# Optimization experiments

Measured on AMD Instinct MI355X. Metric: run time of the kernel, lower is better.

The kernel has to match this reference:

```python
import jax, jax.numpy as jnp
import numpy as np

NUM_HEADS = 16


def rotate_half(x):
    h = x.shape[-1] // 2
    return jnp.concatenate([-x[..., h:], x[..., :h]], axis=-1)


def setup_inputs() -> dict:
    key = jax.random.key(0)
    ks = jax.random.split(key, 8)
    S, dim, hd = 8192, 1280, 80
    n_seg = 8
    hidden_states = jax.random.normal(ks[0], (S, dim), dtype=jnp.float32)
    cu_seqlens = (jnp.arange(n_seg + 1, dtype=jnp.int32) * (S // n_seg))
    ang = jax.random.uniform(ks[1], (S, hd), dtype=jnp.float32) * (2.0 * np.pi)
    cos = jnp.cos(ang)
    sin = jnp.sin(ang)
    qkv_w = jax.random.normal(ks[2], (3 * dim, dim), dtype=jnp.float32) * (dim ** -0.5)
    qkv_b = jax.random.normal(ks[3], (3 * dim,), dtype=jnp.float32) * 0.02
    proj_w = jax.random.normal(ks[4], (dim, dim), dtype=jnp.float32) * (dim ** -0.5)
    proj_b = jax.random.normal(ks[5], (dim,), dtype=jnp.float32) * 0.02
    return {"hidden_states": hidden_states, "cu_seqlens": cu_seqlens,
            "cos": cos, "sin": sin, "qkv_w": qkv_w, "qkv_b": qkv_b,
            "proj_w": proj_w, "proj_b": proj_b}


def reference(hidden_states, cu_seqlens, cos, sin, qkv_w, qkv_b, proj_w, proj_b):
    S, dim = hidden_states.shape
    H = NUM_HEADS
    hd = dim // H
    scaling = hd ** -0.5

    # qkv projection: [S, 3*dim] -> [S, 3, H, hd]
    qkv = (hidden_states @ qkv_w.T + qkv_b).reshape(S, 3, H, hd)
    q, k, v = qkv[:, 0], qkv[:, 1], qkv[:, 2]  # each [S, H, hd]

    # RoPE in float32, cos/sin broadcast over heads
    c = cos[:, None, :].astype(jnp.float32)
    s = sin[:, None, :].astype(jnp.float32)
    qf, kf = q.astype(jnp.float32), k.astype(jnp.float32)
    q = (qf * c + rotate_half(qf) * s).astype(q.dtype)
    k = (kf * c + rotate_half(kf) * s).astype(k.dtype)

    # Block-diagonal varlen attention: equal-length segments -> batch dim
    lengths = np.diff(np.asarray(cu_seqlens))
    L = int(lengths[0])
    assert (lengths == L).all(), "reference assumes uniform segment lengths"
    B = lengths.shape[0]
    qb = q.reshape(B, L, H, hd)
    kb = k.reshape(B, L, H, hd)
    vb = v.reshape(B, L, H, hd)

    scores = jnp.einsum('blhd,bmhd->bhlm', qb, kb) * scaling
    probs = jax.nn.softmax(scores.astype(jnp.float32), axis=-1).astype(scores.dtype)
    out = jnp.einsum('bhlm,bmhd->blhd', probs, vb).reshape(S, dim)

    return out @ proj_w.T + proj_b
```

## Files before the change

### kernel.cpp

```cpp
#include <hip/hip_runtime.h>
#include <math.h>

typedef _Float16 f16;
typedef _Float16 half8 __attribute__((ext_vector_type(8)));
typedef _Float16 half4v __attribute__((ext_vector_type(4)));
typedef _Float16 half2v __attribute__((ext_vector_type(2)));
typedef float floatx4 __attribute__((ext_vector_type(4)));
typedef unsigned int u32;

#define AS1 __attribute__((address_space(1)))
#define AS3 __attribute__((address_space(3)))

__device__ __forceinline__ void stage16(f16* l, const f16* g) {
    __builtin_amdgcn_global_load_lds((const AS1 u32*)g, (AS3 u32*)l, 16, 0, 0);
}

__global__ __launch_bounds__(256) void cvt_f32_f16(const float* __restrict__ in,
                                                   f16* __restrict__ out, int n4) {
    int i = blockIdx.x * blockDim.x + threadIdx.x;
    if (i >= n4) return;
    float4 v = ((const float4*)in)[i];
    half4v h = {(f16)v.x, (f16)v.y, (f16)v.z, (f16)v.w};
    ((half4v*)out)[i] = h;
}

__global__ __launch_bounds__(256) void pack_w(const float* __restrict__ Wf,
                                              f16* __restrict__ Wp) {
    const int p = blockIdx.x * 256 + threadIdx.x;
    const int lane = p & 63;
    const int j = (p >> 6) & 3;
    const int sk = p >> 8;
    const int k0 = sk % 40;
    const int slab = sk / 40;
    const int row = slab * 64 + j * 16 + (lane & 15);
    const int col = k0 * 32 + (lane >> 4) * 8;
    const float* src = Wf + (size_t)row * 1280 + col;
    float4 a = *(const float4*)src;
    float4 b = *(const float4*)(src + 4);
    half8 h = {(f16)a.x, (f16)a.y, (f16)a.z, (f16)a.w,
               (f16)b.x, (f16)b.y, (f16)b.z, (f16)b.w};
    *(half8*)(Wp + (size_t)p * 8) = h;
}

constexpr int GK = 1280;
constexpr int KT = 20;

template <int MT>
__global__ __launch_bounds__(512, 2) void gemm_bp(const f16* __restrict__ A,
                                                  const f16* __restrict__ Bp,
                                                  const float* __restrict__ bias,
                                                  f16* __restrict__ outH,
                                                  float* __restrict__ outF,
                                                  int N, int NT) {
    constexpr int M_FR = MT / 32;
    constexpr int QE = MT * 32;
    __shared__ f16 sm[2][2][QE];
    const int t = threadIdx.x;
    const int lane = t & 63, w = t >> 6;
    const int wm = w >> 2, wn = w & 3;
    const int c16 = lane & 15, quad = lane >> 4;
    const int id = blockIdx.x;
    const int nx = (int)gridDim.x >> 3;
    const int gid = (id & 7) * nx + (id >> 3);
    const int bm = gid / NT, bn = gid - bm * NT;
    const f16* Ab = A + (size_t)bm * MT * GK;
    const f16* Bw = Bp + (size_t)(bn * 4 + wn) * (40 * 4 * 64 * 8) + lane * 8;

    floatx4 acc[M_FR][4] = {};
    half8 bfA[8], bfB[8];

    auto stageA = [&](int kt, int dst) {
#pragma unroll
        for (int ks = 0; ks < 2; ks++)
#pragma unroll
            for (int u = 0; u < MT / 128; u++) {
                const int c = t + u * 512;
                const int row = c >> 2;
                const int lc = ((c & 3) - (row >> 1)) & 3;
                stage16(&sm[dst][ks][0] + c * 8,
                        Ab + (size_t)row * GK + kt * 64 + ks * 32 + lc * 8);
            }
    };
    auto loadB = [&](int kt, half8(&bf)[8]) {
#pragma unroll
        for (int ks = 0; ks < 2; ks++)
#pragma unroll
            for (int j = 0; j < 4; j++)
                bf[ks * 4 + j] = *(const half8*)(Bw + (size_t)((kt * 2 + ks) * 4 + j) * 512);
    };
    auto compute = [&](int p, half8(&bf)[8]) {
#pragma unroll
        for (int ks = 0; ks < 2; ks++) {
            const f16* q = &sm[p][ks][0];
#pragma unroll
            for (int m = 0; m < M_FR; m++) {
                const int r = wm * (MT / 2) + m * 16 + c16;
                half8 a = *(const half8*)(q + r * 32 + (((quad + (r >> 1)) & 3) * 8));
#pragma unroll
                for (int n = 0; n < 4; n++)
                    acc[m][n] = __builtin_amdgcn_mfma_f32_16x16x32_f16(a, bf[ks * 4 + n],
                                                                       acc[m][n], 0, 0, 0);
            }
        }
    };
#define WAIT_STEADY()                                              \
    if constexpr (MT == 256) {                                     \
        asm volatile("s_waitcnt vmcnt(12)" ::: "memory");          \
    } else {                                                       \
        asm volatile("s_waitcnt vmcnt(10)" ::: "memory");          \
    }

    stageA(0, 0);
    loadB(0, bfA);
    asm volatile("s_waitcnt vmcnt(8)" ::: "memory");
    __builtin_amdgcn_s_barrier();

    for (int i = 0; i < 10; i++) {
        const int k0 = 2 * i;
        asm volatile("s_waitcnt lgkmcnt(0)" ::: "memory");
        __builtin_amdgcn_s_barrier();
        stageA(k0 + 1, 1);
        loadB(k0 + 1, bfB);
        WAIT_STEADY();
        __builtin_amdgcn_s_barrier();
        compute(0, bfA);
        asm volatile("s_waitcnt lgkmcnt(0)" ::: "memory");
        __builtin_amdgcn_s_barrier();
        if (i < 9) {
            stageA(k0 + 2, 0);
            loadB(k0 + 2, bfA);
            WAIT_STEADY();
        } else {
            asm volatile("s_waitcnt vmcnt(0)" ::: "memory");
        }
        __builtin_amdgcn_s_barrier();
        compute(1, bfB);
    }

    const int colBase = bn * 256 + wn * 64;
    const size_t rowBase = (size_t)bm * MT + wm * (MT / 2);
    float bv[4];
#pragma unroll
    for (int n = 0; n < 4; n++) bv[n] = bias[colBase + n * 16 + c16];
#pragma unroll
    for (int m = 0; m < M_FR; m++) {
#pragma unroll
        for (int r = 0; r < 4; r++) {
            const size_t row = rowBase + m * 16 + quad * 4 + r;
#pragma unroll
            for (int n = 0; n < 4; n++) {
                const int col = colBase + n * 16 + c16;
                const float v = acc[m][n][r] + bv[n];
                if (outH) outH[row * (size_t)N + col] = (f16)v;
                else      outF[row * (size_t)N + col] = v;
            }
        }
    }
}

__global__ __launch_bounds__(256) void gemm_nt(const f16* __restrict__ A,
                                               const f16* __restrict__ Bp,
                                               const float* __restrict__ bias,
                                               f16* __restrict__ outH,
                                               float* __restrict__ outF, int N) {
    __shared__ f16 As[128 * 32];
    const int t = threadIdx.x;
    const int lane = t & 63;
    const int w = t >> 6;
    const int wm = w & 1, wn = w >> 1;
    const int c16 = lane & 15, quad = lane >> 4;
    const size_t bm = blockIdx.x, bn = blockIdx.y;
    const f16* Ab = A + bm * 128 * GK;
    const f16* Bw = Bp + (size_t)(bn * 2 + wn) * (40 * 4 * 64 * 8);
    floatx4 acc[4][4] = {};
    const int c0 = t, c1 = t + 256;
    const int r0 = c0 >> 2, kc0 = ((c0 & 3) - (r0 >> 1)) & 3;
    const int r1 = c1 >> 2, kc1 = ((c1 & 3) - (r1 >> 1)) & 3;
    for (int k0i = 0; k0i < 40; k0i++) {
        const int k0 = k0i * 32;
        stage16(As + c0 * 8, Ab + (size_t)r0 * GK + k0 + kc0 * 8);
        stage16(As + c1 * 8, Ab + (size_t)r1 * GK + k0 + kc1 * 8);
        half8 bf[4];
#pragma unroll
        for (int j = 0; j < 4; j++)
            bf[j] = *(const half8*)(Bw + (((size_t)k0i * 4 + j) * 64 + lane) * 8);
        __syncthreads();
        half8 af[4];
#pragma unroll
        for (int i = 0; i < 4; i++) {
            const int row = wm * 64 + i * 16 + c16;
            af[i] = *(const half8*)(As + (4 * row + ((quad + (row >> 1)) & 3)) * 8);
        }
#pragma unroll
        for (int i = 0; i < 4; i++)
#pragma unroll
            for (int j = 0; j < 4; j++)
                acc[i][j] = __builtin_amdgcn_mfma_f32_16x16x32_f16(af[i], bf[j], acc[i][j], 0, 0, 0);
        __syncthreads();
    }
#pragma unroll
    for (int i = 0; i < 4; i++) {
#pragma unroll
        for (int j = 0; j < 4; j++) {
            const int col = (int)bn * 128 + wn * 64 + j * 16 + c16;
            const float bv = bias[col];
#pragma unroll
            for (int r = 0; r < 4; r++) {
                const size_t row = bm * 128 + wm * 64 + i * 16 + quad * 4 + r;
                const float v = acc[i][j][r] + bv;
                if (outH) outH[row * (size_t)N + col] = (f16)v;
                else      outF[row * (size_t)N + col] = v;
            }
        }
    }
}

#define QSCALE (0.11180339887498949f * 1.4426950408889634f)

__global__ __launch_bounds__(320) void rope_kernel(const f16* __restrict__ qkv,
                                                   const float* __restrict__ cosp,
                                                   const float* __restrict__ sinp,
                                                   f16* __restrict__ qb, f16* __restrict__ kb,
                                                   f16* __restrict__ vt) {
    constexpr int S = 8192;
    const int bs = blockIdx.x, h = blockIdx.y, t = threadIdx.x;
    const int sl = t / 5, g = t % 5;
    const int s = bs * 64 + sl;
    {
        const size_t base = (size_t)s * 3840 + h * 80 + g * 8;
        half8 qa = *(const half8*)(qkv + base);
        half8 qc = *(const half8*)(qkv + base + 40);
        half8 ka = *(const half8*)(qkv + base + 1280);
        half8 kc = *(const half8*)(qkv + base + 1320);
        const float* cp = cosp + (size_t)s * 80 + g * 8;
        const float* sp = sinp + (size_t)s * 80 + g * 8;
        half8 qo0, qo1, ko0, ko1;
#pragma unroll
        for (int j = 0; j < 8; j++) {
            float c0 = cp[j], c1 = cp[j + 40];
            float n0 = sp[j], n1 = sp[j + 40];
            float q0 = (float)qa[j], q1 = (float)qc[j];
            float k0 = (float)ka[j], k1 = (float)kc[j];
            qo0[j] = (f16)((q0 * c0 - q1 * n0) * QSCALE);
            qo1[j] = (f16)((q1 * c1 + q0 * n1) * QSCALE);
            ko0[j] = (f16)(k0 * c0 - k1 * n0);
            ko1[j] = (f16)(k1 * c1 + k0 * n1);
        }
        const size_t ob = ((size_t)h * S + s) * 96 + g * 8;
        *(half8*)(qb + ob)      = qo0;
        *(half8*)(qb + ob + 40) = qo1;
        *(half8*)(kb + ob)      = ko0;
        *(half8*)(kb + ob + 40) = ko1;
        if (g < 2) {
            half8 qp = {}, kp = {};
            if (g == 0) { qp[0] = (f16)(-8.0f); kp[0] = (f16)(1.0f); }
            const size_t pb = ((size_t)h * S + s) * 96 + 80 + g * 8;
            *(half8*)(qb + pb) = qp;
            *(half8*)(kb + pb) = kp;
        }
    }
    __shared__ f16 vls[64][81];
    for (int j = t; j < 64 * 80; j += 320) {
        int s2 = j / 80, d = j % 80;
        vls[s2][d] = qkv[((size_t)(bs * 64 + s2)) * 3840 + 2560 + h * 80 + d];
    }
    __syncthreads();
    for (int j = t; j < 64 * 80; j += 320) {
        int d = j >> 6, s2 = j & 63;
        vt[((size_t)(h * 80 + d)) * S + bs * 64 + s2] = vls[s2][d];
    }
}

__global__ __launch_bounds__(256, 2) void attn_kernel(const f16* __restrict__ qb,
                                                      const f16* __restrict__ kb,
                                                      const f16* __restrict__ vt,
                                                      const int* __restrict__ cu,
                                                      f16* __restrict__ out) {
    constexpr int S = 8192;
    __shared__ f16 Ks[2][64 * 96];
    __shared__ f16 Ps[256 * 72];
    const int t = threadIdx.x, lane = t & 63, w = t >> 6;
    const int c16 = lane & 15, quad = lane >> 4;
    const int id = blockIdx.x;
    const int pair = id & 127;
    const int qt = id >> 7;
    const int h = pair & 15, z = pair >> 4;
    const int s0 = cu[z];

    half8 qf[4][3];
#pragma unroll
    for (int qt2 = 0; qt2 < 4; qt2++)
#pragma unroll
        for (int ks = 0; ks < 3; ks++)
            qf[qt2][ks] = *(const half8*)(qb + ((size_t)h * S + s0 + qt * 256 + w * 64 + qt2 * 16 + c16) * 96 + ks * 32 + quad * 8);

    const f16 ov = (c16 == 0) ? (f16)1.f : (f16)0.f;
    const half8 onesf = {ov, ov, ov, ov, ov, ov, ov, ov};

    const int sR = t >> 2;
    const int sK = ((t & 3) - (sR >> 1)) & 3;

    {
        const f16* Kg = kb + ((size_t)h * S + s0) * 96;
#pragma unroll
        for (int j = 0; j < 3; j++)
            stage16(&Ks[0][0] + (j * 256 + t) * 8, Kg + (size_t)sR * 96 + j * 32 + sK * 8);
    }
    __syncthreads();

    floatx4 o[6][4] = {};

    for (int kv = 0; kv < 16; kv++) {
        if (kv < 15) {
            const f16* Kg = kb + ((size_t)h * S + s0 + (kv + 1) * 64) * 96;
            f16* Kd = &Ks[(kv + 1) & 1][0];
#pragma unroll
            for (int j = 0; j < 3; j++)
                stage16(Kd + (j * 256 + t) * 8, Kg + (size_t)sR * 96 + j * 32 + sK * 8);
        }
        const f16* Kc = &Ks[kv & 1][0];
        floatx4 sc[4][4] = {};
#pragma unroll
        for (int ks = 0; ks < 3; ks++) {
            half8 kf[4];
#pragma unroll
            for (int mt = 0; mt < 4; mt++) {
                const int row = mt * 16 + c16;
                kf[mt] = *(const half8*)(Kc + (ks * 256 + 4 * row + ((quad + (row >> 1)) & 3)) * 8);
            }
#pragma unroll
            for (int qt2 = 0; qt2 < 4; qt2++)
#pragma unroll
                for (int mt = 0; mt < 4; mt++)
                    sc[mt][qt2] = __builtin_amdgcn_mfma_f32_16x16x32_f16(kf[mt], qf[qt2][ks], sc[mt][qt2], 0, 0, 0);
        }
#pragma unroll
        for (int qt2 = 0; qt2 < 4; qt2++) {
            const int q = w * 64 + qt2 * 16 + c16;
#pragma unroll
            for (int mt = 0; mt < 4; mt++) {
                half4v pv;
#pragma unroll
                for (int r = 0; r < 4; r++)
                    pv[r] = (f16)__builtin_amdgcn_exp2f(sc[mt][qt2][r]);
                *(half4v*)(Ps + q * 72 + mt * 16 + quad * 4) = pv;
            }
        }
#pragma unroll
        for (int ks = 0; ks < 2; ks++) {
            const f16* Vg = vt + (size_t)h * 80 * S + s0 + kv * 64 + ks * 32;
            half8 vf[5];
#pragma unroll
            for (int dt = 0; dt < 5; dt++)
                vf[dt] = *(const half8*)(Vg + (size_t)(dt * 16 + c16) * S + quad * 8);
#pragma unroll
            for (int qt2 = 0; qt2 < 4; qt2++) {
                const int q = w * 64 + qt2 * 16 + c16;
                half8 pf = *(const half8*)(Ps + q * 72 + ks * 32 + quad * 8);
#pragma unroll
                for (int dt = 0; dt < 5; dt++)
                    o[dt][qt2] = __builtin_amdgcn_mfma_f32_16x16x32_f16(vf[dt], pf, o[dt][qt2], 0, 0, 0);
                o[5][qt2] = __builtin_amdgcn_mfma_f32_16x16x32_f16(onesf, pf, o[5][qt2], 0, 0, 0);
            }
        }
        __syncthreads();
    }
#pragma unroll
    for (int qt2 = 0; qt2 < 4; qt2++) {
        const float l = __shfl(o[5][qt2][0], c16);
        const float inv = 1.f / l;
        const size_t srow = (size_t)s0 + qt * 256 + w * 64 + qt2 * 16 + c16;
#pragma unroll
        for (int dt = 0; dt < 5; dt++)
#pragma unroll
            for (int rp = 0; rp < 2; rp++) {
                half2v hv = {(f16)(o[dt][qt2][rp * 2] * inv), (f16)(o[dt][qt2][rp * 2 + 1] * inv)};
                *(half2v*)(out + srow * 1280 + h * 80 + dt * 16 + quad * 4 + rp * 2) = hv;
            }
    }
}

extern "C" void kernel_launch(void* const* d_in, const int* in_sizes, int n_in,
                              void* d_out, int out_size, void* d_ws, size_t ws_size,
                              hipStream_t stream) {
    const float* hidden = (const float*)d_in[0];
    const int* cu       = (const int*)d_in[1];
    const float* cosp   = (const float*)d_in[2];
    const float* sinp   = (const float*)d_in[3];
    const float* qkv_w  = (const float*)d_in[4];
    const float* qkv_b  = (const float*)d_in[5];
    const float* proj_w = (const float*)d_in[6];
    const float* proj_b = (const float*)d_in[7];
    float* out = (float*)d_out;

    constexpr size_t S = 8192, DIM = 1280, N3 = 3840;
    f16* A16   = (f16*)d_ws;
    f16* WP16  = A16 + S * DIM;
    f16* PP16  = WP16 + N3 * DIM;
    f16* QKV16 = PP16 + DIM * DIM;
    f16* QB    = QKV16 + S * N3;
    f16* KB    = QB + (size_t)16 * S * 96;
    f16* VT    = KB + (size_t)16 * S * 96;
    f16* AT16  = A16;

    {
        int n4 = (int)(S * DIM / 4);
        cvt_f32_f16<<<(n4 + 255) / 256, 256, 0, stream>>>(hidden, A16, n4);
    }
    pack_w<<<(int)(N3 * DIM / 8 / 256), 256, 0, stream>>>(qkv_w, WP16);
    pack_w<<<(int)(DIM * DIM / 8 / 256), 256, 0, stream>>>(proj_w, PP16);
    gemm_bp<256><<<16 * 15, 512, 0, stream>>>(A16, WP16, qkv_b, QKV16, nullptr, 3840, 15);
    gemm_bp<256><<<16 * 15, 512, 0, stream>>>(A16 + (size_t)16 * 256 * GK, WP16, qkv_b,
                                              QKV16 + (size_t)16 * 256 * 3840, nullptr, 3840, 15);
    rope_kernel<<<dim3(128, 16), 320, 0, stream>>>(QKV16, cosp, sinp, QB, KB, VT);
    attn_kernel<<<512, 256, 0, stream>>>(QB, KB, VT, cu, A16);
    gemm_nt<<<dim3(64, 10), 256, 0, stream>>>(AT16, PP16, proj_b, nullptr, out, 1280);
}
```

Measured before the change: 364.6 us.

## Split attention KV tile into halves with per-wave swizzled P buffer

The score, exp and PV stages are restructured to run over two 32-key halves of each 64-key tile instead of computing all scores first. Each wave now has its own swizzled 64x32 probability buffer in LDS, and a lane-dependent half swap on read undoes the swizzle. This shrinks the score register footprint and LDS usage and is meant to cut bank conflicts on the P writes and reads. The cost is extra select instructions and more interleaved K and V loads per half.

```diff
diff --git a/kernel.cpp b/kernel.cpp
--- a/kernel.cpp
+++ b/kernel.cpp
@@ -278,7 +278,7 @@
                                                       f16* __restrict__ out) {
     constexpr int S = 8192;
     __shared__ f16 Ks[2][64 * 96];
-    __shared__ f16 Ps[256 * 72];
+    __shared__ f16 Ps[4][64 * 32];
     const int t = threadIdx.x, lane = t & 63, w = t >> 6;
     const int c16 = lane & 15, quad = lane >> 4;
     const int id = blockIdx.x;
@@ -309,6 +309,10 @@
     __syncthreads();
 
     floatx4 o[6][4] = {};
+    const int swW = (c16 >> 1) & 3;
+    const int subW = (quad & 1) ^ ((c16 >> 3) & 1);
+    const bool rdsw = (c16 & 8) != 0;
+    f16* Pw = &Ps[w][0];
 
     for (int kv = 0; kv < 16; kv++) {
         if (kv < 15) {
@@ -319,44 +323,51 @@
                 stage16(Kd + (j * 256 + t) * 8, Kg + (size_t)sR * 96 + j * 32 + sK * 8);
         }
         const f16* Kc = &Ks[kv & 1][0];
-        floatx4 sc[4][4] = {};
-#pragma unroll
-        for (int ks = 0; ks < 3; ks++) {
-            half8 kf[4];
-#pragma unroll
-            for (int mt = 0; mt < 4; mt++) {
-                const int row = mt * 16 + c16;
-                kf[mt] = *(const half8*)(Kc + (ks * 256 + 4 * row + ((quad + (row >> 1)) & 3)) * 8);
-            }
-#pragma unroll
-            for (int qt2 = 0; qt2 < 4; qt2++)
-#pragma unroll
-                for (int mt = 0; mt < 4; mt++)
-                    sc[mt][qt2] = __builtin_amdgcn_mfma_f32_16x16x32_f16(kf[mt], qf[qt2][ks], sc[mt][qt2], 0, 0, 0);
-        }
-#pragma unroll
-        for (int qt2 = 0; qt2 < 4; qt2++) {
-            const int q = w * 64 + qt2 * 16 + c16;
-#pragma unroll
-            for (int mt = 0; mt < 4; mt++) {
-                half4v pv;
-#pragma unroll
-                for (int r = 0; r < 4; r++)
-                    pv[r] = (f16)__builtin_amdgcn_exp2f(sc[mt][qt2][r]);
-                *(half4v*)(Ps + q * 72 + mt * 16 + quad * 4) = pv;
-            }
-        }
-#pragma unroll
-        for (int ks = 0; ks < 2; ks++) {
-            const f16* Vg = vt + (size_t)h * 80 * S + s0 + kv * 64 + ks * 32;
+#pragma unroll
+        for (int hs = 0; hs < 2; hs++) {
             half8 vf[5];
+            const f16* Vg = vt + (size_t)h * 80 * S + s0 + kv * 64 + hs * 32;
 #pragma unroll
             for (int dt = 0; dt < 5; dt++)
                 vf[dt] = *(const half8*)(Vg + (size_t)(dt * 16 + c16) * S + quad * 8);
+            floatx4 sc[2][4] = {};
+#pragma unroll
+            for (int ks = 0; ks < 3; ks++) {
+                half8 kf[2];
+#pragma unroll
+                for (int mtl = 0; mtl < 2; mtl++) {
+                    const int row = (hs * 2 + mtl) * 16 + c16;
+                    kf[mtl] = *(const half8*)(Kc + (ks * 256 + 4 * row + ((quad + (row >> 1)) & 3)) * 8);
+                }
+#pragma unroll
+                for (int qt2 = 0; qt2 < 4; qt2++)
+#pragma unroll
+                    for (int mtl = 0; mtl < 2; mtl++)
+                        sc[mtl][qt2] = __builtin_amdgcn_mfma_f32_16x16x32_f16(kf[mtl], qf[qt2][ks], sc[mtl][qt2], 0, 0, 0);
+            }
 #pragma unroll
             for (int qt2 = 0; qt2 < 4; qt2++) {
-                const int q = w * 64 + qt2 * 16 + c16;
-                half8 pf = *(const half8*)(Ps + q * 72 + ks * 32 + quad * 8);
+                const int ql = qt2 * 16 + c16;
+#pragma unroll
+                for (int mtl = 0; mtl < 2; mtl++) {
+                    half4v pv;
+#pragma unroll
+                    for (int r = 0; r < 4; r++)
+                        pv[r] = (f16)__builtin_amdgcn_exp2f(sc[mtl][qt2][r]);
+                    const int phys = ((mtl * 2 + (quad >> 1)) + swW) & 3;
+                    *(half4v*)(Pw + ql * 32 + phys * 8 + subW * 4) = pv;
+                }
+            }
+#pragma unroll
+            for (int qt2 = 0; qt2 < 4; qt2++) {
+                const int ql = qt2 * 16 + c16;
+                half8 raw = *(const half8*)(Pw + ql * 32 + (((quad + swW) & 3) * 8));
+                half8 pf;
+#pragma unroll
+                for (int j = 0; j < 4; j++) {
+                    pf[j]     = rdsw ? raw[j + 4] : raw[j];
+                    pf[j + 4] = rdsw ? raw[j]     : raw[j + 4];
+                }
 #pragma unroll
                 for (int dt = 0; dt < 5; dt++)
                     o[dt][qt2] = __builtin_amdgcn_mfma_f32_16x16x32_f16(vf[dt], pf, o[dt][qt2], 0, 0, 0);
```

Result: no change. 371.8 us (+2.0%).
